# Optimization experiments

Hardware: AMD Instinct MI355X
Metric: run time of the kernel (lower is better)

Reference implementation:

```python
import jax, jax.numpy as jnp
import numpy as np

# All unordered pairs of 6 ligand sites (octahedral complex)
PAIRS = np.array([(i, j) for i in range(6) for j in range(i + 1, 6)], dtype=np.int32)  # [15, 2]

B, N_LIGS, D = 32768, 6, 64
IN_DIM = D + 2 * D  # core + lig_i + lig_j = 192
H1, H2 = 64, 32


def setup_inputs() -> dict:
    key = jax.random.key(0)
    ks = jax.random.split(key, 8)
    s = 0.05  # small init scale for numerical sanity
    return {
        "core": jax.random.normal(ks[0], (B, D), dtype=jnp.float32),
        "ligs": jax.random.normal(ks[1], (B, N_LIGS, D), dtype=jnp.float32),
        "W1": jax.random.normal(ks[2], (IN_DIM, H1), dtype=jnp.float32) * s,
        "b1": jnp.zeros((H1,), dtype=jnp.float32),
        "W2": jax.random.normal(ks[3], (H1, H2), dtype=jnp.float32) * s,
        "b2": jnp.zeros((H2,), dtype=jnp.float32),
        "W3": jax.random.normal(ks[4], (H2, 1), dtype=jnp.float32) * s,
        "b3": jnp.zeros((1,), dtype=jnp.float32),
    }


def _mlp(x, W1, b1, W2, b2, W3, b3):
    # Dense(softplus) -> Dense(softplus) -> Dense(1, linear); dropout is identity at inference
    h = jax.nn.softplus(x @ W1 + b1)
    h = jax.nn.softplus(h @ W2 + b2)
    return h @ W3 + b3  # [..., 1]


def reference(core, ligs, W1, b1, W2, b2, W3, b3):
    i_idx = jnp.asarray(PAIRS[:, 0])
    j_idx = jnp.asarray(PAIRS[:, 1])
    P = PAIRS.shape[0]
    li = ligs[:, i_idx, :]  # [B, P, D]
    lj = ligs[:, j_idx, :]  # [B, P, D]
    c = jnp.broadcast_to(core[:, None, :], (core.shape[0], P, core.shape[1]))
    x1 = jnp.concatenate([c, li, lj], axis=-1)  # [B, P, 3D]
    x2 = jnp.concatenate([c, lj, li], axis=-1)  # [B, P, 3D]
    res = 0.5 * (_mlp(x1, W1, b1, W2, b2, W3, b3) + _mlp(x2, W1, b1, W2, b2, W3, b3))  # [B, P, 1]
    return jnp.sum(res, axis=1)  # [B, 1]
```

## Files before the change

### kernel.cpp

```cpp
#include <hip/hip_runtime.h>
#include <stdint.h>


typedef __attribute__((ext_vector_type(8))) short bf16x8;
typedef __attribute__((ext_vector_type(4))) float f32x4;
typedef __attribute__((ext_vector_type(4))) unsigned int u32x4;

constexpr int   BPB      = 64;
constexpr int   NT       = 1024;
constexpr int   T_STRIDE = 1680;
constexpr int   WT_RS    = 72;
constexpr int   WT_OFF   = BPB * T_STRIDE;
constexpr int   W2T_OFF  = WT_OFF + 192 * WT_RS * 2;
constexpr int   XB_OFF   = W2T_OFF + 32 * WT_RS * 2;
constexpr int   Y_OFF    = XB_OFF + 64 * WT_RS * 2;
constexpr int   LDS_BYTES = Y_OFF + 256;

constexpr float L2E = 1.4426950408889634f;
constexpr float LN2 = 0.6931471805599453f;

constexpr unsigned long long I_BITS =
  (0ull<<0)|(0ull<<3)|(0ull<<6)|(0ull<<9)|(0ull<<12)|
  (1ull<<15)|(1ull<<18)|(1ull<<21)|(1ull<<24)|
  (2ull<<27)|(2ull<<30)|(2ull<<33)|
  (3ull<<36)|(3ull<<39)|(4ull<<42);
constexpr unsigned long long J_BITS =
  (1ull<<0)|(2ull<<3)|(3ull<<6)|(4ull<<9)|(5ull<<12)|
  (2ull<<15)|(3ull<<18)|(4ull<<21)|(5ull<<24)|
  (3ull<<27)|(4ull<<30)|(5ull<<33)|
  (4ull<<36)|(5ull<<39)|(5ull<<42);

__device__ __forceinline__ uint32_t bf16_rn(float f) {
  union { float f; uint32_t u; } v; v.f = f;
  uint32_t u = v.u;
  return (u + 0x7fffu + ((u >> 16) & 1u)) >> 16;
}

__device__ __forceinline__ void unpk2(uint32_t d, float& lo, float& hi) {
  union { uint32_t u; float f; } a, b;
  a.u = d << 16; b.u = d & 0xffff0000u;
  lo = a.f; hi = b.f;
}

__device__ __forceinline__ float sp2(float s) {
  float t = __builtin_amdgcn_exp2f(s);
  return __builtin_amdgcn_logf(1.0f + t);
}

__device__ __forceinline__ uint32_t sp2pair(uint32_t du, uint32_t da, uint32_t db) {
  float u0, u1, a0, a1, v0, v1;
  unpk2(du, u0, u1); unpk2(da, a0, a1); unpk2(db, v0, v1);
  float h0 = sp2(u0 + a0 + v0);
  float h1 = sp2(u1 + a1 + v1);
  return bf16_rn(h0) | (bf16_rn(h1) << 16);
}

__global__ __launch_bounds__(NT, 4)
void tb_fused(const float* __restrict__ core, const float* __restrict__ ligs,
              const float* __restrict__ W1,   const float* __restrict__ b1,
              const float* __restrict__ W2,   const float* __restrict__ b2,
              const float* __restrict__ W3,   const float* __restrict__ b3,
              float* __restrict__ out)
{
  extern __shared__ char smem[];
  const int tid  = (int)threadIdx.x;
  const int lane = tid & 63;
  const int ln   = lane & 15;
  const int qd   = lane >> 4;
  const int wv   = __builtin_amdgcn_readfirstlane(tid >> 6);
  const int b0   = (int)blockIdx.x * BPB;

  float* yred = (float*)(smem + Y_OFF);

  for (int idx = tid; idx < 12288; idx += NT) {
    const int d = idx >> 6, n = idx & 63;
    *(uint16_t*)(smem + WT_OFF + ((((d >> 6) * 64 + n) * WT_RS + (d & 63)) * 2)) =
        (uint16_t)bf16_rn(W1[idx] * L2E);
  }
  for (int idx = tid; idx < 2048; idx += NT) {
    const int k = idx >> 5, m = idx & 31;
    *(uint16_t*)(smem + W2T_OFF + ((m * WT_RS + k) * 2)) =
        (uint16_t)bf16_rn(W2[idx] * (LN2 * L2E));
  }
  if (tid < 64) yred[tid] = 0.0f;
  __syncthreads();

  bf16x8 W2f[2][2];
  #pragma unroll
  for (int nt = 0; nt < 2; ++nt)
    #pragma unroll
    for (int ks = 0; ks < 2; ++ks)
      W2f[nt][ks] = *(const bf16x8*)(smem + W2T_OFF +
          (((nt * 16 + ln) * WT_RS + ks * 32 + qd * 8) * 2));

  float b2v[2], w3v[2];
  #pragma unroll
  for (int nt = 0; nt < 2; ++nt) {
    b2v[nt] = b2[nt * 16 + ln] * L2E;
    w3v[nt] = W3[nt * 16 + ln] * LN2;
  }

  auto p1_unit = [&](int slab, int mt, int nt, int trow, bool add_b1) {
    f32x4 c = {0.f, 0.f, 0.f, 0.f};
    #pragma unroll
    for (int ks = 0; ks < 2; ++ks) {
      bf16x8 A = *(const bf16x8*)(smem + XB_OFF +
          (((mt * 16 + ln) * WT_RS + ks * 32 + qd * 8) * 2));
      bf16x8 Bf = *(const bf16x8*)(smem + WT_OFF +
          (((slab * 64 + nt * 16 + ln) * WT_RS + ks * 32 + qd * 8) * 2));
      c = __builtin_amdgcn_mfma_f32_16x16x32_bf16(A, Bf, c, 0, 0, 0);
    }
    const float bias = add_b1 ? b1[nt * 16 + ln] * L2E : 0.0f;
    #pragma unroll
    for (int reg = 0; reg < 4; ++reg) {
      const int b = mt * 16 + qd * 4 + reg;
      *(uint16_t*)(smem + (size_t)b * T_STRIDE + trow * 128 + (nt * 16 + ln) * 2) =
          (uint16_t)bf16_rn(c[reg] + bias);
    }
  };

  #pragma unroll 1
  for (int xr = 0; xr < 7; ++xr) {
    if (tid < 512) {
      const int b = tid >> 3, d0 = (tid & 7) * 8;
      const float* src = (xr == 0)
          ? (core + (size_t)(b0 + b) * 64 + d0)
          : (ligs + ((size_t)(b0 + b) * 6 + (size_t)(xr - 1)) * 64 + d0);
      const float4 f0 = *(const float4*)(src);
      const float4 f1 = *(const float4*)(src + 4);
      u32x4 pk;
      pk.x = bf16_rn(f0.x) | (bf16_rn(f0.y) << 16);
      pk.y = bf16_rn(f0.z) | (bf16_rn(f0.w) << 16);
      pk.z = bf16_rn(f1.x) | (bf16_rn(f1.y) << 16);
      pk.w = bf16_rn(f1.z) | (bf16_rn(f1.w) << 16);
      *(u32x4*)(smem + XB_OFF + ((b * WT_RS + d0) * 2)) = pk;
    }
    __syncthreads();

    if (xr == 0) {
      p1_unit(0, wv >> 2, wv & 3, 0, true);
    } else {
      p1_unit(1, wv >> 2, wv & 3, xr, false);
      p1_unit(2, wv >> 2, wv & 3, 6 + xr, false);
    }
    __syncthreads();
  }

  float yacc[16];
  #pragma unroll
  for (int i = 0; i < 16; ++i) yacc[i] = 0.0f;

  #pragma unroll 1
  for (int u = wv; u < 120; u += 16) {
    const int q  = u >> 2;
    const int mt = u & 3;
    const int p  = q >> 1;
    const int iv = (int)((I_BITS >> (3 * p)) & 7ull);
    const int jv = (int)((J_BITS >> (3 * p)) & 7ull);
    const int An = (q & 1) ? jv : iv;
    const int Bn = (q & 1) ? iv : jv;

    const char* Tb = smem + (size_t)(mt * 16 + ln) * T_STRIDE;
    const int rA = (1 + An) * 128;
    const int rB = (7 + Bn) * 128;

    f32x4 c0 = {0.f, 0.f, 0.f, 0.f};
    f32x4 c1 = {0.f, 0.f, 0.f, 0.f};
    #pragma unroll
    for (int ks = 0; ks < 2; ++ks) {
      const int koff = (ks * 32 + qd * 8) * 2;
      const u32x4 du = *(const u32x4*)(Tb + koff);
      const u32x4 da = *(const u32x4*)(Tb + rA + koff);
      const u32x4 db = *(const u32x4*)(Tb + rB + koff);
      union { u32x4 u; bf16x8 v; } A;
      A.u.x = sp2pair(du.x, da.x, db.x);
      A.u.y = sp2pair(du.y, da.y, db.y);
      A.u.z = sp2pair(du.z, da.z, db.z);
      A.u.w = sp2pair(du.w, da.w, db.w);
      c0 = __builtin_amdgcn_mfma_f32_16x16x32_bf16(A.v, W2f[0][ks], c0, 0, 0, 0);
      c1 = __builtin_amdgcn_mfma_f32_16x16x32_bf16(A.v, W2f[1][ks], c1, 0, 0, 0);
    }
    #pragma unroll
    for (int reg = 0; reg < 4; ++reg) {
      float y = sp2(c0[reg] + b2v[0]) * w3v[0]
              + sp2(c1[reg] + b2v[1]) * w3v[1];
      yacc[mt * 4 + reg] += y;
    }
  }

  #pragma unroll
  for (int i = 0; i < 16; ++i) {
    float v = yacc[i];
    v += __shfl_xor(v, 1);
    v += __shfl_xor(v, 2);
    v += __shfl_xor(v, 4);
    v += __shfl_xor(v, 8);
    yacc[i] = v;
  }
  if (ln == 0) {
    #pragma unroll
    for (int mt = 0; mt < 4; ++mt)
      #pragma unroll
      for (int reg = 0; reg < 4; ++reg)
        atomicAdd(&yred[mt * 16 + qd * 4 + reg], yacc[mt * 4 + reg]);
  }
  __syncthreads();
  if (tid < 64) out[b0 + tid] = 0.5f * yred[tid] + 15.0f * b3[0];
}

extern "C" void kernel_launch(void* const* d_in, const int* in_sizes, int n_in,
                              void* d_out, int out_size, void* d_ws, size_t ws_size,
                              hipStream_t stream) {
  const float* core = (const float*)d_in[0];
  const float* ligs = (const float*)d_in[1];
  const float* W1   = (const float*)d_in[2];
  const float* b1   = (const float*)d_in[3];
  const float* W2   = (const float*)d_in[4];
  const float* b2   = (const float*)d_in[5];
  const float* W3   = (const float*)d_in[6];
  const float* b3   = (const float*)d_in[7];
  float* out = (float*)d_out;

  const int B = in_sizes[0] / 64;
  const int grid = B / BPB;

  (void)hipFuncSetAttribute((const void*)tb_fused,
                            hipFuncAttributeMaxDynamicSharedMemorySize, LDS_BYTES);

  tb_fused<<<dim3(grid), dim3(NT), LDS_BYTES, stream>>>(
      core, ligs, W1, b1, W2, b2, W3, b3, out);
}
```

Before: 146.8 us.

## Switch to fp16 MFMA with packed half2 softplus and direct-register input loads

Replaces bf16 with fp16 for weights, layer-1 outputs and MFMA inputs. The first-layer softplus now runs as packed half2 exp2/log2, which roughly halves the transcendental and conversion work. Inputs are loaded straight from global memory into MFMA A fragments, dropping the staging LDS buffer and the 14 per-row barriers. Work is also remapped so each wave owns a fixed row tile, which shrinks the accumulators to four registers. fp16 arithmetic in the softplus, with W2 no longer prescaled, raises the risk of precision loss or overflow.

After: 126.9 us. -13.6%, faster.

```diff
diff --git a/kernel.cpp b/kernel.cpp
--- a/kernel.cpp
+++ b/kernel.cpp
@@ -1,9 +1,11 @@
 #include <hip/hip_runtime.h>
+#include <hip/hip_fp16.h>
 #include <stdint.h>
 
 
-typedef __attribute__((ext_vector_type(8))) short bf16x8;
-typedef __attribute__((ext_vector_type(4))) float f32x4;
+typedef __attribute__((ext_vector_type(8))) _Float16 f16x8;
+typedef __attribute__((ext_vector_type(2))) __fp16   fp16v2;
+typedef __attribute__((ext_vector_type(4))) float    f32x4;
 typedef __attribute__((ext_vector_type(4))) unsigned int u32x4;
 
 constexpr int   BPB      = 64;
@@ -12,8 +14,7 @@
 constexpr int   WT_RS    = 72;
 constexpr int   WT_OFF   = BPB * T_STRIDE;
 constexpr int   W2T_OFF  = WT_OFF + 192 * WT_RS * 2;
-constexpr int   XB_OFF   = W2T_OFF + 32 * WT_RS * 2;
-constexpr int   Y_OFF    = XB_OFF + 64 * WT_RS * 2;
+constexpr int   Y_OFF    = W2T_OFF + 32 * WT_RS * 2;
 constexpr int   LDS_BYTES = Y_OFF + 256;
 
 constexpr float L2E = 1.4426950408889634f;
@@ -30,29 +31,16 @@
   (3ull<<27)|(4ull<<30)|(5ull<<33)|
   (4ull<<36)|(5ull<<39)|(5ull<<42);
 
-__device__ __forceinline__ uint32_t bf16_rn(float f) {
-  union { float f; uint32_t u; } v; v.f = f;
-  uint32_t u = v.u;
-  return (u + 0x7fffu + ((u >> 16) & 1u)) >> 16;
-}
-
-__device__ __forceinline__ void unpk2(uint32_t d, float& lo, float& hi) {
-  union { uint32_t u; float f; } a, b;
-  a.u = d << 16; b.u = d & 0xffff0000u;
-  lo = a.f; hi = b.f;
-}
-
 __device__ __forceinline__ float sp2(float s) {
   float t = __builtin_amdgcn_exp2f(s);
   return __builtin_amdgcn_logf(1.0f + t);
 }
 
-__device__ __forceinline__ uint32_t sp2pair(uint32_t du, uint32_t da, uint32_t db) {
-  float u0, u1, a0, a1, v0, v1;
-  unpk2(du, u0, u1); unpk2(da, a0, a1); unpk2(db, v0, v1);
-  float h0 = sp2(u0 + a0 + v0);
-  float h1 = sp2(u1 + a1 + v1);
-  return bf16_rn(h0) | (bf16_rn(h1) << 16);
+__device__ __forceinline__ __half2 h1pair(__half2 u, __half2 a, __half2 b,
+                                          __half2 one2) {
+  __half2 s = __hadd2(__hadd2(u, a), b);
+  __half2 t = h2exp2(s);
+  return h2log2(__hadd2(one2, t));
 }
 
 __global__ __launch_bounds__(NT, 4)
@@ -68,29 +56,78 @@
   const int ln   = lane & 15;
   const int qd   = lane >> 4;
   const int wv   = __builtin_amdgcn_readfirstlane(tid >> 6);
+  const int qr   = wv >> 2;
+  const int mtw  = wv & 3;
   const int b0   = (int)blockIdx.x * BPB;
 
   float* yred = (float*)(smem + Y_OFF);
 
+  #pragma unroll 4
   for (int idx = tid; idx < 12288; idx += NT) {
     const int d = idx >> 6, n = idx & 63;
     *(uint16_t*)(smem + WT_OFF + ((((d >> 6) * 64 + n) * WT_RS + (d & 63)) * 2)) =
-        (uint16_t)bf16_rn(W1[idx] * L2E);
-  }
+        __half_as_ushort(__float2half(W1[idx] * L2E));
+  }
+  #pragma unroll
   for (int idx = tid; idx < 2048; idx += NT) {
     const int k = idx >> 5, m = idx & 31;
     *(uint16_t*)(smem + W2T_OFF + ((m * WT_RS + k) * 2)) =
-        (uint16_t)bf16_rn(W2[idx] * (LN2 * L2E));
+        __half_as_ushort(__float2half(W2[idx]));
   }
   if (tid < 64) yred[tid] = 0.0f;
   __syncthreads();
 
-  bf16x8 W2f[2][2];
+  #pragma unroll 1
+  for (int rep = 0; rep < 2; ++rep) {
+    const int xr = qr + rep * 4;
+    if (xr >= 7) break;
+    const float* src = (xr == 0)
+        ? (core + (size_t)(b0 + mtw * 16 + ln) * 64)
+        : (ligs + ((size_t)(b0 + mtw * 16 + ln) * 6 + (size_t)(xr - 1)) * 64);
+
+    union AF { f16x8 v; fp16v2 p[4]; } Afr[2];
+    #pragma unroll
+    for (int ks = 0; ks < 2; ++ks) {
+      const float4 f0 = *(const float4*)(src + ks * 32 + qd * 8);
+      const float4 f1 = *(const float4*)(src + ks * 32 + qd * 8 + 4);
+      Afr[ks].p[0] = __builtin_amdgcn_cvt_pkrtz(f0.x, f0.y);
+      Afr[ks].p[1] = __builtin_amdgcn_cvt_pkrtz(f0.z, f0.w);
+      Afr[ks].p[2] = __builtin_amdgcn_cvt_pkrtz(f1.x, f1.y);
+      Afr[ks].p[3] = __builtin_amdgcn_cvt_pkrtz(f1.z, f1.w);
+    }
+
+    const int sl_lo = (xr == 0) ? 0 : 1;
+    const int sl_hi = (xr == 0) ? 0 : 2;
+    #pragma unroll 1
+    for (int sl = sl_lo; sl <= sl_hi; ++sl) {
+      const int trow = (xr == 0) ? 0 : ((sl == 1) ? xr : 6 + xr);
+      #pragma unroll
+      for (int nt = 0; nt < 4; ++nt) {
+        f32x4 c = {0.f, 0.f, 0.f, 0.f};
+        #pragma unroll
+        for (int ks = 0; ks < 2; ++ks) {
+          f16x8 Bf = *(const f16x8*)(smem + WT_OFF +
+              (((sl * 64 + nt * 16 + ln) * WT_RS + ks * 32 + qd * 8) * 2));
+          c = __builtin_amdgcn_mfma_f32_16x16x32_f16(Afr[ks].v, Bf, c, 0, 0, 0);
+        }
+        const float bias = (xr == 0) ? b1[nt * 16 + ln] * L2E : 0.0f;
+        #pragma unroll
+        for (int reg = 0; reg < 4; ++reg) {
+          const int b = mtw * 16 + qd * 4 + reg;
+          *(uint16_t*)(smem + (size_t)b * T_STRIDE + trow * 128 + (nt * 16 + ln) * 2) =
+              __half_as_ushort(__float2half(c[reg] + bias));
+        }
+      }
+    }
+  }
+  __syncthreads();
+
+  f16x8 W2f[2][2];
   #pragma unroll
   for (int nt = 0; nt < 2; ++nt)
     #pragma unroll
     for (int ks = 0; ks < 2; ++ks)
-      W2f[nt][ks] = *(const bf16x8*)(smem + W2T_OFF +
+      W2f[nt][ks] = *(const f16x8*)(smem + W2T_OFF +
           (((nt * 16 + ln) * WT_RS + ks * 32 + qd * 8) * 2));
 
   float b2v[2], w3v[2];
@@ -100,109 +137,66 @@
     w3v[nt] = W3[nt * 16 + ln] * LN2;
   }
 
-  auto p1_unit = [&](int slab, int mt, int nt, int trow, bool add_b1) {
-    f32x4 c = {0.f, 0.f, 0.f, 0.f};
-    #pragma unroll
-    for (int ks = 0; ks < 2; ++ks) {
-      bf16x8 A = *(const bf16x8*)(smem + XB_OFF +
-          (((mt * 16 + ln) * WT_RS + ks * 32 + qd * 8) * 2));
-      bf16x8 Bf = *(const bf16x8*)(smem + WT_OFF +
-          (((slab * 64 + nt * 16 + ln) * WT_RS + ks * 32 + qd * 8) * 2));
-      c = __builtin_amdgcn_mfma_f32_16x16x32_bf16(A, Bf, c, 0, 0, 0);
-    }
-    const float bias = add_b1 ? b1[nt * 16 + ln] * L2E : 0.0f;
-    #pragma unroll
-    for (int reg = 0; reg < 4; ++reg) {
-      const int b = mt * 16 + qd * 4 + reg;
-      *(uint16_t*)(smem + (size_t)b * T_STRIDE + trow * 128 + (nt * 16 + ln) * 2) =
-          (uint16_t)bf16_rn(c[reg] + bias);
-    }
-  };
-
-  #pragma unroll 1
-  for (int xr = 0; xr < 7; ++xr) {
-    if (tid < 512) {
-      const int b = tid >> 3, d0 = (tid & 7) * 8;
-      const float* src = (xr == 0)
-          ? (core + (size_t)(b0 + b) * 64 + d0)
-          : (ligs + ((size_t)(b0 + b) * 6 + (size_t)(xr - 1)) * 64 + d0);
-      const float4 f0 = *(const float4*)(src);
-      const float4 f1 = *(const float4*)(src + 4);
-      u32x4 pk;
-      pk.x = bf16_rn(f0.x) | (bf16_rn(f0.y) << 16);
-      pk.y = bf16_rn(f0.z) | (bf16_rn(f0.w) << 16);
-      pk.z = bf16_rn(f1.x) | (bf16_rn(f1.y) << 16);
-      pk.w = bf16_rn(f1.z) | (bf16_rn(f1.w) << 16);
-      *(u32x4*)(smem + XB_OFF + ((b * WT_RS + d0) * 2)) = pk;
-    }
-    __syncthreads();
-
-    if (xr == 0) {
-      p1_unit(0, wv >> 2, wv & 3, 0, true);
-    } else {
-      p1_unit(1, wv >> 2, wv & 3, xr, false);
-      p1_unit(2, wv >> 2, wv & 3, 6 + xr, false);
-    }
-    __syncthreads();
-  }
-
-  float yacc[16];
-  #pragma unroll
-  for (int i = 0; i < 16; ++i) yacc[i] = 0.0f;
-
-  #pragma unroll 1
-  for (int u = wv; u < 120; u += 16) {
-    const int q  = u >> 2;
-    const int mt = u & 3;
+  const __half2 one2 = __float2half2_rn(1.0f);
+  const char* Tb  = smem + (size_t)(mtw * 16 + ln) * T_STRIDE;
+  const int koff  = qd * 16;
+
+  float yacc[4] = {0.f, 0.f, 0.f, 0.f};
+
+  #pragma unroll 2
+  for (int t3 = 0; t3 < 8; ++t3) {
+    const int q = qr + 4 * t3;
+    if (q >= 30) break;
     const int p  = q >> 1;
     const int iv = (int)((I_BITS >> (3 * p)) & 7ull);
     const int jv = (int)((J_BITS >> (3 * p)) & 7ull);
     const int An = (q & 1) ? jv : iv;
     const int Bn = (q & 1) ? iv : jv;
-
-    const char* Tb = smem + (size_t)(mt * 16 + ln) * T_STRIDE;
-    const int rA = (1 + An) * 128;
-    const int rB = (7 + Bn) * 128;
+    const char* TA = Tb + (1 + An) * 128;
+    const char* TB = Tb + (7 + Bn) * 128;
+
+    union U4 { u32x4 u; __half2 h[4]; };
+    U4 du0, da0, db0, du1, da1, db1;
+    du0.u = *(const u32x4*)(Tb + koff);
+    da0.u = *(const u32x4*)(TA + koff);
+    db0.u = *(const u32x4*)(TB + koff);
+    du1.u = *(const u32x4*)(Tb + 64 + koff);
+    da1.u = *(const u32x4*)(TA + 64 + koff);
+    db1.u = *(const u32x4*)(TB + 64 + koff);
+
+    union { f16x8 v; __half2 h[4]; } A0, A1;
+    #pragma unroll
+    for (int w = 0; w < 4; ++w) A0.h[w] = h1pair(du0.h[w], da0.h[w], db0.h[w], one2);
+    #pragma unroll
+    for (int w = 0; w < 4; ++w) A1.h[w] = h1pair(du1.h[w], da1.h[w], db1.h[w], one2);
 
     f32x4 c0 = {0.f, 0.f, 0.f, 0.f};
     f32x4 c1 = {0.f, 0.f, 0.f, 0.f};
-    #pragma unroll
-    for (int ks = 0; ks < 2; ++ks) {
-      const int koff = (ks * 32 + qd * 8) * 2;
-      const u32x4 du = *(const u32x4*)(Tb + koff);
-      const u32x4 da = *(const u32x4*)(Tb + rA + koff);
-      const u32x4 db = *(const u32x4*)(Tb + rB + koff);
-      union { u32x4 u; bf16x8 v; } A;
-      A.u.x = sp2pair(du.x, da.x, db.x);
-      A.u.y = sp2pair(du.y, da.y, db.y);
-      A.u.z = sp2pair(du.z, da.z, db.z);
-      A.u.w = sp2pair(du.w, da.w, db.w);
-      c0 = __builtin_amdgcn_mfma_f32_16x16x32_bf16(A.v, W2f[0][ks], c0, 0, 0, 0);
-      c1 = __builtin_amdgcn_mfma_f32_16x16x32_bf16(A.v, W2f[1][ks], c1, 0, 0, 0);
+    c0 = __builtin_amdgcn_mfma_f32_16x16x32_f16(A0.v, W2f[0][0], c0, 0, 0, 0);
+    c0 = __builtin_amdgcn_mfma_f32_16x16x32_f16(A1.v, W2f[0][1], c0, 0, 0, 0);
+    c1 = __builtin_amdgcn_mfma_f32_16x16x32_f16(A0.v, W2f[1][0], c1, 0, 0, 0);
+    c1 = __builtin_amdgcn_mfma_f32_16x16x32_f16(A1.v, W2f[1][1], c1, 0, 0, 0);
+
+    #pragma unroll
+    for (int reg = 0; reg < 4; ++reg) {
+      yacc[reg] += sp2(c0[reg] + b2v[0]) * w3v[0]
+                 + sp2(c1[reg] + b2v[1]) * w3v[1];
     }
-    #pragma unroll
-    for (int reg = 0; reg < 4; ++reg) {
-      float y = sp2(c0[reg] + b2v[0]) * w3v[0]
-              + sp2(c1[reg] + b2v[1]) * w3v[1];
-      yacc[mt * 4 + reg] += y;
-    }
-  }
-
-  #pragma unroll
-  for (int i = 0; i < 16; ++i) {
-    float v = yacc[i];
+  }
+
+  #pragma unroll
+  for (int reg = 0; reg < 4; ++reg) {
+    float v = yacc[reg];
     v += __shfl_xor(v, 1);
     v += __shfl_xor(v, 2);
     v += __shfl_xor(v, 4);
     v += __shfl_xor(v, 8);
-    yacc[i] = v;
+    yacc[reg] = v;
   }
   if (ln == 0) {
     #pragma unroll
-    for (int mt = 0; mt < 4; ++mt)
-      #pragma unroll
-      for (int reg = 0; reg < 4; ++reg)
-        atomicAdd(&yred[mt * 16 + qd * 4 + reg], yacc[mt * 4 + reg]);
+    for (int reg = 0; reg < 4; ++reg)
+      atomicAdd(&yred[mtw * 16 + qd * 4 + reg], yacc[reg]);
   }
   __syncthreads();
   if (tid < 64) out[b0 + tid] = 0.5f * yred[tid] + 15.0f * b3[0];
```
